# Kernel optimization log

Hardware: AMD Instinct MI355X
Metric: run time of the kernel (lower is better)

Reference implementation:

```python
import jax, jax.numpy as jnp
import numpy as np

G = 8      # n_group
P = 32     # input channels per group (256 // 8)
F = 64     # filters per group
KH = KW = 3
CIN = G * P   # 256
COUT = G * F  # 512


def setup_inputs() -> dict:
    key = jax.random.key(0)
    k1, k2, k3 = jax.random.split(key, 3)
    x = jax.random.normal(k1, (16, 56, 56, CIN), dtype=jnp.float32)
    kernels = jax.random.normal(k2, (G, KH, KW, P, F), dtype=jnp.float32) * 0.05
    bias = jax.random.normal(k3, (COUT,), dtype=jnp.float32) * 0.05
    return {"x": x, "kernels": kernels, "bias": bias}


def _build_dense_kernel(kernels):
    # Faithful to build_weights_for_group_conv: zero-pad each group's kernel
    # along the input-channel axis to full width, then concat along output
    # channels -> block-diagonal dense kernel [KH, KW, CIN, COUT].
    w = jnp.zeros((KH, KW, CIN, COUT), dtype=kernels.dtype)
    for i in range(G):
        w = w.at[:, :, i * P:(i + 1) * P, i * F:(i + 1) * F].set(kernels[i])
    return w


def reference(x, kernels, bias):
    w = _build_dense_kernel(kernels)
    # Single dense cuDNN-style conv over the zero-padded block-diagonal kernel,
    # exactly as tf.nn.convolution(inputs, w, strides, 'SAME', dilations).
    out = jax.lax.conv_general_dilated(
        x, w,
        window_strides=(1, 1),
        padding='SAME',
        rhs_dilation=(1, 1),
        dimension_numbers=('NHWC', 'HWIO', 'NHWC'),
    )
    return out + bias
```

## Files before the change

### kernel.cpp

```cpp
#include <hip/hip_runtime.h>

#define NG 8
#define PC 32
#define FC 64
#define HH 56
#define WW 56
#define CIN 256
#define COUT 512
#define NB 16
#define SL 66
#define PLANE (SL * 64)
#define NPL 5
#define PLF (64 * 128)
#define HCH 7

typedef __bf16 bf16x8 __attribute__((ext_vector_type(8)));
typedef float f32x4 __attribute__((ext_vector_type(4)));

static __device__ __forceinline__ void dma16(const void* gsrc, void* lds) {
    typedef const __attribute__((address_space(1))) unsigned int* gp_t;
    typedef __attribute__((address_space(3))) unsigned int* lp_t;
    __builtin_amdgcn_global_load_lds((gp_t)gsrc, (lp_t)lds, 16, 0, 0);
}

static __device__ __forceinline__ bf16x8 cvt8(f32x4 a, f32x4 b) {
    bf16x8 r;
    r[0] = (__bf16)a[0]; r[1] = (__bf16)a[1]; r[2] = (__bf16)a[2]; r[3] = (__bf16)a[3];
    r[4] = (__bf16)b[0]; r[5] = (__bf16)b[1]; r[6] = (__bf16)b[2]; r[7] = (__bf16)b[3];
    return r;
}

static __device__ __forceinline__ int swz(int loc) {
    return loc ^ (((loc >> 7) & 3) << 4);
}
static __device__ __forceinline__ int swz32(int loc) {
    return loc ^ (((loc >> 7) & 7) << 4);
}

__global__ __launch_bounds__(256, 4)
void groupconv_onew_kernel(const float* __restrict__ x,
                           const float* __restrict__ krn,
                           const float* __restrict__ bias,
                           float* __restrict__ out) {
    const int b   = blockIdx.x;
    const int g   = b & 7;
    const int hcb = (b >> 3) & 7;
    const int n   = b >> 6;
    const int h0  = hcb * HCH;

    const int tid  = threadIdx.x;
    const int wave = tid >> 6;
    const int lane = tid & 63;
    const int lo = lane & 15;
    const int hi = lane >> 4;
    const int p0 = hi * 8;
    const int fm  = (wave >> 1) * 32;
    const int wnb = (wave & 1) * 32;

    __shared__ __align__(16) unsigned char lds[2 * PLF + NPL * PLANE];
    unsigned char* const F0 = lds;
    unsigned char* const F1 = lds + PLF;
    unsigned char* const Bb = lds + 2 * PLF;

    {
        const float* kg = krn + (size_t)g * (9 * PC * FC);
#pragma unroll
        for (int k = 0; k < 18; ++k) {
            const int u  = tid + k * 256;
            const int fq = u & 15;
            const int p  = (u >> 4) & 31;
            const int t  = u >> 9;
            f32x4 v = *reinterpret_cast<const f32x4*>(kg + ((size_t)t * PC + p) * FC + fq * 4);
            const int gr = (p >> 3) ^ (fq & 3);
            __bf16* wp = reinterpret_cast<__bf16*>(
                lds + ((t * 64 + fq * 4) * 64) + gr * 16 + (p & 7) * 2);
#pragma unroll
            for (int j = 0; j < 4; ++j)
                wp[j * 32] = (__bf16)v[j];
        }
    }
    __syncthreads();

    bf16x8 bfr[9][2];
    {
        const int gx = hi ^ ((lo >> 2) & 3);
#pragma unroll
        for (int t = 0; t < 9; ++t)
#pragma unroll
            for (int mi = 0; mi < 2; ++mi) {
                const int f = fm + mi * 16 + lo;
                bfr[t][mi] = *reinterpret_cast<const bf16x8*>(
                    lds + (t * 64 + f) * 64 + gx * 16);
            }
    }
    __syncthreads();

    const int o0 = tid * 16,        o1 = (tid + 256) * 16;
    const int l0 = swz32(o0),       l1 = swz32(o1);
    const int s0 = l0 >> 7,         s1 = l1 >> 7;
    const int q0 = (l0 >> 4) & 7,   q1 = (l1 >> 4) & 7;
    const bool ok0 = (s0 >= 1 && s0 <= 56);
    const bool ok1 = (s1 >= 1 && s1 <= 56);
    const float* xg = x + ((size_t)n * HH * WW) * CIN + g * PC;
    const size_t off0 = (size_t)(s0 - 1) * CIN + q0 * 4;
    const size_t off1 = (size_t)(s1 - 1) * CIN + q1 * 4;

    const int sc  = tid >> 2;
    const int qc  = tid & 3;
    const int frd = swz32(sc * 128 + qc * 32);
    const int bwr = swz(sc * 64 + qc * 16);

    if (!ok0) { *reinterpret_cast<f32x4*>(F0 + o0) = (f32x4)0.f;
                *reinterpret_cast<f32x4*>(F1 + o0) = (f32x4)0.f; }
    if (!ok1) { *reinterpret_cast<f32x4*>(F0 + o1) = (f32x4)0.f;
                *reinterpret_cast<f32x4*>(F1 + o1) = (f32x4)0.f; }
    if (tid < 180) {
        const int q  = tid & 3;
        const int sq = tid >> 2;
        const int pl = sq / 9;
        const int s  = 57 + (sq % 9);
        *reinterpret_cast<bf16x8*>(Bb + pl * PLANE + swz(s * 64 + q * 16)) =
            (bf16x8)(__bf16)0.f;
    }

#define STAGE(r_, Fdst)                                                         \
    do {                                                                        \
        const int r__ = (r_);                                                   \
        if ((unsigned)r__ < HH) {                                               \
            const float* rowp__ = xg + (size_t)r__ * WW * CIN;                  \
            if (ok0) dma16(rowp__ + off0, (Fdst) + wave * 1024);                \
            if (ok1) dma16(rowp__ + off1, (Fdst) + 4096 + wave * 1024);         \
        } else {                                                                \
            if (ok0) *reinterpret_cast<f32x4*>((Fdst) + o0) = (f32x4)0.f;       \
            if (ok1) *reinterpret_cast<f32x4*>((Fdst) + o1) = (f32x4)0.f;       \
        }                                                                       \
    } while (0)

#define CVTROW(Fsrc, Bdst)                                                      \
    do {                                                                        \
        f32x4 a__  = *reinterpret_cast<const f32x4*>((Fsrc) + frd);             \
        f32x4 b2__ = *reinterpret_cast<const f32x4*>((Fsrc) + (frd ^ 16));      \
        *reinterpret_cast<bf16x8*>((Bdst) + bwr) = cvt8(a__, b2__);             \
    } while (0)

    STAGE(h0 - 1, F0);
    STAGE(h0,     F1);
    asm volatile("s_waitcnt vmcnt(0) lgkmcnt(0)\n\ts_barrier" ::: "memory");
    CVTROW(F0, Bb + 0 * PLANE);
    CVTROW(F1, Bb + 1 * PLANE);
    asm volatile("s_waitcnt lgkmcnt(0)\n\ts_barrier" ::: "memory");
    STAGE(h0 + 1, F0);
    asm volatile("s_waitcnt vmcnt(0) lgkmcnt(0)\n\ts_barrier" ::: "memory");
    CVTROW(F0, Bb + 2 * PLANE);
    asm volatile("s_waitcnt lgkmcnt(0)\n\ts_barrier" ::: "memory");
    STAGE(h0 + 2, F0);

    float4 bvv[2];
#pragma unroll
    for (int mi = 0; mi < 2; ++mi)
        bvv[mi] = *reinterpret_cast<const float4*>(bias + g * FC + fm + mi * 16 + hi * 4);

    float* const outg = out + ((size_t)n * HH * WW) * COUT + g * FC;

#pragma unroll
    for (int i = 0; i < HCH; ++i) {
        const int h = h0 + i;

        if (i == 0)
            asm volatile("s_waitcnt vmcnt(0) lgkmcnt(0)\n\ts_barrier" ::: "memory");
        else
            asm volatile("s_waitcnt vmcnt(4) lgkmcnt(0)\n\ts_barrier" ::: "memory");

        if (i <= HCH - 2) {
            const unsigned char* Fsrc = (i & 1) ? F1 : F0;
            CVTROW(Fsrc, Bb + ((i + 3) % NPL) * PLANE);
        }
        if (i <= HCH - 3) {
            unsigned char* Fdst = ((i + 1) & 1) ? F1 : F0;
            STAGE(h + 3, Fdst);
        }

        f32x4 acc[2][2];
#pragma unroll
        for (int mi = 0; mi < 2; ++mi)
#pragma unroll
            for (int nj = 0; nj < 2; ++nj) acc[mi][nj] = (f32x4)0.f;

#pragma unroll
        for (int kh = 0; kh < 3; ++kh) {
            const unsigned char* plb = Bb + ((i + kh) % NPL) * PLANE;
#pragma unroll
            for (int kw = 0; kw < 3; ++kw) {
                const int t = kh * 3 + kw;
                bf16x8 bx[2];
#pragma unroll
                for (int nj = 0; nj < 2; ++nj) {
                    const int ss = wnb + nj * 16 + lo + kw;
                    bx[nj] = *reinterpret_cast<const bf16x8*>(plb + swz(ss * 64 + hi * 16));
                }
#pragma unroll
                for (int mi = 0; mi < 2; ++mi)
#pragma unroll
                    for (int nj = 0; nj < 2; ++nj)
                        acc[mi][nj] = __builtin_amdgcn_mfma_f32_16x16x32_bf16(
                            bfr[t][mi], bx[nj], acc[mi][nj], 0, 0, 0);
            }
        }

        float* const orow = outg + ((size_t)h * WW) * COUT;
#pragma unroll
        for (int mi = 0; mi < 2; ++mi) {
            const int f0 = fm + mi * 16 + hi * 4;
#pragma unroll
            for (int nj = 0; nj < 2; ++nj) {
                const int w = wnb + nj * 16 + lo;
                if (w < WW) {
                    f32x4 oo = acc[mi][nj];
                    oo[0] += bvv[mi].x; oo[1] += bvv[mi].y;
                    oo[2] += bvv[mi].z; oo[3] += bvv[mi].w;
                    *reinterpret_cast<f32x4*>(orow + (size_t)w * COUT + f0) = oo;
                }
            }
        }
    }
#undef STAGE
#undef CVTROW
}

extern "C" void kernel_launch(void* const* d_in, const int* in_sizes, int n_in,
                              void* d_out, int out_size, void* d_ws, size_t ws_size,
                              hipStream_t stream) {
    const float* x    = (const float*)d_in[0];
    const float* krn  = (const float*)d_in[1];
    const float* bias = (const float*)d_in[2];
    float* out = (float*)d_out;

    const int blocks = NB * 8 * NG;
    groupconv_onew_kernel<<<blocks, 256, 0, stream>>>(x, krn, bias, out);
}
```

Baseline: 36.52 us.

## Shrink LDS footprint and row chunk to raise occupancy with more blocks

Cuts the LDS plane width and the number of planes, and stages the weights in two passes so the staging region fits in less LDS. Each block now covers 4 output rows instead of 7, giving 14 chunks per image and more blocks in the grid. Launch bounds go from 4 to 5 blocks per SIMD. Out-of-range column reads are clamped to the last plane column, which is only valid if the zero padding still holds, and the shorter row chunk means more redundant halo row loads and conversions per block.

Measured after the change: 76.82 us. +110.3%, slower.

```diff
diff --git a/kernel.cpp b/kernel.cpp
--- a/kernel.cpp
+++ b/kernel.cpp
@@ -8,11 +8,12 @@
 #define CIN 256
 #define COUT 512
 #define NB 16
-#define SL 66
+#define SL 58
 #define PLANE (SL * 64)
-#define NPL 5
+#define NPL 4
 #define PLF (64 * 128)
-#define HCH 7
+#define HCH 4
+#define NCH 14
 
 typedef __bf16 bf16x8 __attribute__((ext_vector_type(8)));
 typedef float f32x4 __attribute__((ext_vector_type(4)));
@@ -37,15 +38,15 @@
     return loc ^ (((loc >> 7) & 7) << 4);
 }
 
-__global__ __launch_bounds__(256, 4)
-void groupconv_onew_kernel(const float* __restrict__ x,
+__global__ __launch_bounds__(256, 5)
+void groupconv_slim_kernel(const float* __restrict__ x,
                            const float* __restrict__ krn,
                            const float* __restrict__ bias,
                            float* __restrict__ out) {
     const int b   = blockIdx.x;
     const int g   = b & 7;
-    const int hcb = (b >> 3) & 7;
-    const int n   = b >> 6;
+    const int hcb = (b >> 3) % NCH;
+    const int n   = b / (8 * NCH);
     const int h0  = hcb * HCH;
 
     const int tid  = threadIdx.x;
@@ -53,7 +54,6 @@
     const int lane = tid & 63;
     const int lo = lane & 15;
     const int hi = lane >> 4;
-    const int p0 = hi * 8;
     const int fm  = (wave >> 1) * 32;
     const int wnb = (wave & 1) * 32;
 
@@ -62,10 +62,12 @@
     unsigned char* const F1 = lds + PLF;
     unsigned char* const Bb = lds + 2 * PLF;
 
+    bf16x8 bfr[9][2];
     {
         const float* kg = krn + (size_t)g * (9 * PC * FC);
-#pragma unroll
-        for (int k = 0; k < 18; ++k) {
+        const int gx = hi ^ ((lo >> 2) & 3);
+#pragma unroll
+        for (int k = 0; k < 10; ++k) {
             const int u  = tid + k * 256;
             const int fq = u & 15;
             const int p  = (u >> 4) & 31;
@@ -75,25 +77,39 @@
             __bf16* wp = reinterpret_cast<__bf16*>(
                 lds + ((t * 64 + fq * 4) * 64) + gr * 16 + (p & 7) * 2);
 #pragma unroll
-            for (int j = 0; j < 4; ++j)
-                wp[j * 32] = (__bf16)v[j];
-        }
+            for (int j = 0; j < 4; ++j) wp[j * 32] = (__bf16)v[j];
+        }
+        __syncthreads();
+#pragma unroll
+        for (int t = 0; t < 5; ++t)
+#pragma unroll
+            for (int mi = 0; mi < 2; ++mi)
+                bfr[t][mi] = *reinterpret_cast<const bf16x8*>(
+                    lds + (t * 64 + fm + mi * 16 + lo) * 64 + gx * 16);
+        __syncthreads();
+#pragma unroll
+        for (int k = 0; k < 8; ++k) {
+            const int u  = tid + k * 256;
+            const int fq = u & 15;
+            const int p  = (u >> 4) & 31;
+            const int t5 = u >> 9;
+            f32x4 v = *reinterpret_cast<const f32x4*>(
+                kg + ((size_t)(t5 + 5) * PC + p) * FC + fq * 4);
+            const int gr = (p >> 3) ^ (fq & 3);
+            __bf16* wp = reinterpret_cast<__bf16*>(
+                lds + ((t5 * 64 + fq * 4) * 64) + gr * 16 + (p & 7) * 2);
+#pragma unroll
+            for (int j = 0; j < 4; ++j) wp[j * 32] = (__bf16)v[j];
+        }
+        __syncthreads();
+#pragma unroll
+        for (int t5 = 0; t5 < 4; ++t5)
+#pragma unroll
+            for (int mi = 0; mi < 2; ++mi)
+                bfr[t5 + 5][mi] = *reinterpret_cast<const bf16x8*>(
+                    lds + (t5 * 64 + fm + mi * 16 + lo) * 64 + gx * 16);
+        __syncthreads();
     }
-    __syncthreads();
-
-    bf16x8 bfr[9][2];
-    {
-        const int gx = hi ^ ((lo >> 2) & 3);
-#pragma unroll
-        for (int t = 0; t < 9; ++t)
-#pragma unroll
-            for (int mi = 0; mi < 2; ++mi) {
-                const int f = fm + mi * 16 + lo;
-                bfr[t][mi] = *reinterpret_cast<const bf16x8*>(
-                    lds + (t * 64 + f) * 64 + gx * 16);
-            }
-    }
-    __syncthreads();
 
     const int o0 = tid * 16,        o1 = (tid + 256) * 16;
     const int l0 = swz32(o0),       l1 = swz32(o1);
@@ -109,19 +125,12 @@
     const int qc  = tid & 3;
     const int frd = swz32(sc * 128 + qc * 32);
     const int bwr = swz(sc * 64 + qc * 16);
+    const bool cvt_ok = (sc < SL);
 
     if (!ok0) { *reinterpret_cast<f32x4*>(F0 + o0) = (f32x4)0.f;
                 *reinterpret_cast<f32x4*>(F1 + o0) = (f32x4)0.f; }
     if (!ok1) { *reinterpret_cast<f32x4*>(F0 + o1) = (f32x4)0.f;
                 *reinterpret_cast<f32x4*>(F1 + o1) = (f32x4)0.f; }
-    if (tid < 180) {
-        const int q  = tid & 3;
-        const int sq = tid >> 2;
-        const int pl = sq / 9;
-        const int s  = 57 + (sq % 9);
-        *reinterpret_cast<bf16x8*>(Bb + pl * PLANE + swz(s * 64 + q * 16)) =
-            (bf16x8)(__bf16)0.f;
-    }
 
 #define STAGE(r_, Fdst)                                                         \
     do {                                                                        \
@@ -138,9 +147,11 @@
 
 #define CVTROW(Fsrc, Bdst)                                                      \
     do {                                                                        \
-        f32x4 a__  = *reinterpret_cast<const f32x4*>((Fsrc) + frd);             \
-        f32x4 b2__ = *reinterpret_cast<const f32x4*>((Fsrc) + (frd ^ 16));      \
-        *reinterpret_cast<bf16x8*>((Bdst) + bwr) = cvt8(a__, b2__);             \
+        if (cvt_ok) {                                                           \
+            f32x4 a__  = *reinterpret_cast<const f32x4*>((Fsrc) + frd);         \
+            f32x4 b2__ = *reinterpret_cast<const f32x4*>((Fsrc) + (frd ^ 16));  \
+            *reinterpret_cast<bf16x8*>((Bdst) + bwr) = cvt8(a__, b2__);         \
+        }                                                                       \
     } while (0)
 
     STAGE(h0 - 1, F0);
@@ -195,7 +206,8 @@
                 bf16x8 bx[2];
 #pragma unroll
                 for (int nj = 0; nj < 2; ++nj) {
-                    const int ss = wnb + nj * 16 + lo + kw;
+                    int ss = wnb + nj * 16 + lo + kw;
+                    ss = (ss > 57) ? 57 : ss;
                     bx[nj] = *reinterpret_cast<const bf16x8*>(plb + swz(ss * 64 + hi * 16));
                 }
 #pragma unroll
@@ -235,6 +247,6 @@
     const float* bias = (const float*)d_in[2];
     float* out = (float*)d_out;
 
-    const int blocks = NB * 8 * NG;
-    groupconv_onew_kernel<<<blocks, 256, 0, stream>>>(x, krn, bias, out);
-}
+    const int blocks = NB * NCH * NG;
+    groupconv_slim_kernel<<<blocks, 256, 0, stream>>>(x, krn, bias, out);
+}
```

## Overlap first input-row DMAs with split weight staging in LDS

Applied to the files above, without the earlier changes.

Issues the first two input-row async loads before weight preparation, and stages the weights in two halves through the bf16 plane buffer region so they don't collide with the fp32 staging buffers. It also issues the fourth row's load earlier and flips the ping-pong buffer assignment to match. The aim is to hide global load latency in the prologue behind the weight conversion. The cost is extra barriers and a second weight pass.

After: 39.54 us. 8.3% more time.

```diff
diff --git a/kernel.cpp b/kernel.cpp
--- a/kernel.cpp
+++ b/kernel.cpp
@@ -38,10 +38,10 @@
 }
 
 __global__ __launch_bounds__(256, 4)
-void groupconv_onew_kernel(const float* __restrict__ x,
-                           const float* __restrict__ krn,
-                           const float* __restrict__ bias,
-                           float* __restrict__ out) {
+void groupconv_ovl_kernel(const float* __restrict__ x,
+                          const float* __restrict__ krn,
+                          const float* __restrict__ bias,
+                          float* __restrict__ out) {
     const int b   = blockIdx.x;
     const int g   = b & 7;
     const int hcb = (b >> 3) & 7;
@@ -53,7 +53,6 @@
     const int lane = tid & 63;
     const int lo = lane & 15;
     const int hi = lane >> 4;
-    const int p0 = hi * 8;
     const int fm  = (wave >> 1) * 32;
     const int wnb = (wave & 1) * 32;
 
@@ -61,39 +60,6 @@
     unsigned char* const F0 = lds;
     unsigned char* const F1 = lds + PLF;
     unsigned char* const Bb = lds + 2 * PLF;
-
-    {
-        const float* kg = krn + (size_t)g * (9 * PC * FC);
-#pragma unroll
-        for (int k = 0; k < 18; ++k) {
-            const int u  = tid + k * 256;
-            const int fq = u & 15;
-            const int p  = (u >> 4) & 31;
-            const int t  = u >> 9;
-            f32x4 v = *reinterpret_cast<const f32x4*>(kg + ((size_t)t * PC + p) * FC + fq * 4);
-            const int gr = (p >> 3) ^ (fq & 3);
-            __bf16* wp = reinterpret_cast<__bf16*>(
-                lds + ((t * 64 + fq * 4) * 64) + gr * 16 + (p & 7) * 2);
-#pragma unroll
-            for (int j = 0; j < 4; ++j)
-                wp[j * 32] = (__bf16)v[j];
-        }
-    }
-    __syncthreads();
-
-    bf16x8 bfr[9][2];
-    {
-        const int gx = hi ^ ((lo >> 2) & 3);
-#pragma unroll
-        for (int t = 0; t < 9; ++t)
-#pragma unroll
-            for (int mi = 0; mi < 2; ++mi) {
-                const int f = fm + mi * 16 + lo;
-                bfr[t][mi] = *reinterpret_cast<const bf16x8*>(
-                    lds + (t * 64 + f) * 64 + gx * 16);
-            }
-    }
-    __syncthreads();
 
     const int o0 = tid * 16,        o1 = (tid + 256) * 16;
     const int l0 = swz32(o0),       l1 = swz32(o1);
@@ -104,6 +70,71 @@
     const float* xg = x + ((size_t)n * HH * WW) * CIN + g * PC;
     const size_t off0 = (size_t)(s0 - 1) * CIN + q0 * 4;
     const size_t off1 = (size_t)(s1 - 1) * CIN + q1 * 4;
+
+#define STAGE(r_, Fdst)                                                         \
+    do {                                                                        \
+        const int r__ = (r_);                                                   \
+        if ((unsigned)r__ < HH) {                                               \
+            const float* rowp__ = xg + (size_t)r__ * WW * CIN;                  \
+            if (ok0) dma16(rowp__ + off0, (Fdst) + wave * 1024);                \
+            if (ok1) dma16(rowp__ + off1, (Fdst) + 4096 + wave * 1024);         \
+        } else {                                                                \
+            if (ok0) *reinterpret_cast<f32x4*>((Fdst) + o0) = (f32x4)0.f;       \
+            if (ok1) *reinterpret_cast<f32x4*>((Fdst) + o1) = (f32x4)0.f;       \
+        }                                                                       \
+    } while (0)
+
+    STAGE(h0 - 1, F0);
+    STAGE(h0,     F1);
+
+    bf16x8 bfr[9][2];
+    {
+        const float* kg = krn + (size_t)g * (9 * PC * FC);
+        const int gx = hi ^ ((lo >> 2) & 3);
+#pragma unroll
+        for (int k = 0; k < 10; ++k) {
+            const int u  = tid + k * 256;
+            const int fq = u & 15;
+            const int p  = (u >> 4) & 31;
+            const int t  = u >> 9;
+            f32x4 v = *reinterpret_cast<const f32x4*>(kg + ((size_t)t * PC + p) * FC + fq * 4);
+            const int gr = (p >> 3) ^ (fq & 3);
+            __bf16* wp = reinterpret_cast<__bf16*>(
+                Bb + ((t * 64 + fq * 4) * 64) + gr * 16 + (p & 7) * 2);
+#pragma unroll
+            for (int j = 0; j < 4; ++j) wp[j * 32] = (__bf16)v[j];
+        }
+        __syncthreads();
+#pragma unroll
+        for (int t = 0; t < 5; ++t)
+#pragma unroll
+            for (int mi = 0; mi < 2; ++mi)
+                bfr[t][mi] = *reinterpret_cast<const bf16x8*>(
+                    Bb + (t * 64 + fm + mi * 16 + lo) * 64 + gx * 16);
+        __syncthreads();
+#pragma unroll
+        for (int k = 0; k < 8; ++k) {
+            const int u  = tid + k * 256;
+            const int fq = u & 15;
+            const int p  = (u >> 4) & 31;
+            const int t5 = u >> 9;
+            f32x4 v = *reinterpret_cast<const f32x4*>(
+                kg + ((size_t)(t5 + 5) * PC + p) * FC + fq * 4);
+            const int gr = (p >> 3) ^ (fq & 3);
+            __bf16* wp = reinterpret_cast<__bf16*>(
+                Bb + ((t5 * 64 + fq * 4) * 64) + gr * 16 + (p & 7) * 2);
+#pragma unroll
+            for (int j = 0; j < 4; ++j) wp[j * 32] = (__bf16)v[j];
+        }
+        __syncthreads();
+#pragma unroll
+        for (int t5 = 0; t5 < 4; ++t5)
+#pragma unroll
+            for (int mi = 0; mi < 2; ++mi)
+                bfr[t5 + 5][mi] = *reinterpret_cast<const bf16x8*>(
+                    Bb + (t5 * 64 + fm + mi * 16 + lo) * 64 + gx * 16);
+        __syncthreads();
+    }
 
     const int sc  = tid >> 2;
     const int qc  = tid & 3;
@@ -123,19 +154,6 @@
             (bf16x8)(__bf16)0.f;
     }
 
-#define STAGE(r_, Fdst)                                                         \
-    do {                                                                        \
-        const int r__ = (r_);                                                   \
-        if ((unsigned)r__ < HH) {                                               \
-            const float* rowp__ = xg + (size_t)r__ * WW * CIN;                  \
-            if (ok0) dma16(rowp__ + off0, (Fdst) + wave * 1024);                \
-            if (ok1) dma16(rowp__ + off1, (Fdst) + 4096 + wave * 1024);         \
-        } else {                                                                \
-            if (ok0) *reinterpret_cast<f32x4*>((Fdst) + o0) = (f32x4)0.f;       \
-            if (ok1) *reinterpret_cast<f32x4*>((Fdst) + o1) = (f32x4)0.f;       \
-        }                                                                       \
-    } while (0)
-
 #define CVTROW(Fsrc, Bdst)                                                      \
     do {                                                                        \
         f32x4 a__  = *reinterpret_cast<const f32x4*>((Fsrc) + frd);             \
@@ -143,17 +161,14 @@
         *reinterpret_cast<bf16x8*>((Bdst) + bwr) = cvt8(a__, b2__);             \
     } while (0)
 
-    STAGE(h0 - 1, F0);
-    STAGE(h0,     F1);
     asm volatile("s_waitcnt vmcnt(0) lgkmcnt(0)\n\ts_barrier" ::: "memory");
     CVTROW(F0, Bb + 0 * PLANE);
     CVTROW(F1, Bb + 1 * PLANE);
     asm volatile("s_waitcnt lgkmcnt(0)\n\ts_barrier" ::: "memory");
     STAGE(h0 + 1, F0);
+    STAGE(h0 + 2, F1);
     asm volatile("s_waitcnt vmcnt(0) lgkmcnt(0)\n\ts_barrier" ::: "memory");
     CVTROW(F0, Bb + 2 * PLANE);
-    asm volatile("s_waitcnt lgkmcnt(0)\n\ts_barrier" ::: "memory");
-    STAGE(h0 + 2, F0);
 
     float4 bvv[2];
 #pragma unroll
@@ -172,11 +187,11 @@
             asm volatile("s_waitcnt vmcnt(4) lgkmcnt(0)\n\ts_barrier" ::: "memory");
 
         if (i <= HCH - 2) {
-            const unsigned char* Fsrc = (i & 1) ? F1 : F0;
+            const unsigned char* Fsrc = (i & 1) ? F0 : F1;
             CVTROW(Fsrc, Bb + ((i + 3) % NPL) * PLANE);
         }
         if (i <= HCH - 3) {
-            unsigned char* Fdst = ((i + 1) & 1) ? F1 : F0;
+            unsigned char* Fdst = (i & 1) ? F1 : F0;
             STAGE(h + 3, Fdst);
         }
 
@@ -236,5 +251,5 @@
     float* out = (float*)d_out;
 
     const int blocks = NB * 8 * NG;
-    groupconv_onew_kernel<<<blocks, 256, 0, stream>>>(x, krn, bias, out);
-}
+    groupconv_ovl_kernel<<<blocks, 256, 0, stream>>>(x, krn, bias, out);
+}
```
